# Performance work log

Hardware: AMD Instinct MI355X
Metric: run time of the kernel (lower is better)

## Reference

```python
import jax, jax.numpy as jnp
import numpy as np

HEADS = 16
D_MODEL = 1024
D_K = D_MODEL // HEADS


def setup_inputs() -> dict:
    key = jax.random.key(0)
    ks = jax.random.split(key, 11)
    B, S, D = 4, 2048, D_MODEL
    q = jax.random.normal(ks[0], (B, S, D), dtype=jnp.float32)
    k = jax.random.normal(ks[1], (B, S, D), dtype=jnp.float32)
    v = jax.random.normal(ks[2], (B, S, D), dtype=jnp.float32)
    s = 1.0 / np.sqrt(D)
    Wq = jax.random.normal(ks[3], (D, D), dtype=jnp.float32) * s
    bq = jax.random.normal(ks[4], (D,), dtype=jnp.float32) * 0.01
    Wk = jax.random.normal(ks[5], (D, D), dtype=jnp.float32) * s
    bk = jax.random.normal(ks[6], (D,), dtype=jnp.float32) * 0.01
    Wv = jax.random.normal(ks[7], (D, D), dtype=jnp.float32) * s
    bv = jax.random.normal(ks[8], (D,), dtype=jnp.float32) * 0.01
    Wo = jax.random.normal(ks[9], (D, D), dtype=jnp.float32) * s
    bo = jax.random.normal(ks[10], (D,), dtype=jnp.float32) * 0.01
    return {"q": q, "k": k, "v": v, "Wq": Wq, "bq": bq, "Wk": Wk, "bk": bk,
            "Wv": Wv, "bv": bv, "Wo": Wo, "bo": bo}


def reference(q, k, v, Wq, bq, Wk, bk, Wv, bv, Wo, bo):
    B, Sq, D = q.shape
    Sk = k.shape[1]
    # Linear projections (torch Linear: x @ W.T + b)
    q_ = (q @ Wq.T + bq).reshape(B, Sq, HEADS, D_K).transpose(0, 2, 1, 3)  # [B,H,Sq,Dk]
    k_ = (k @ Wk.T + bk).reshape(B, Sk, HEADS, D_K).transpose(0, 2, 1, 3)  # [B,H,Sk,Dk]
    v_ = (v @ Wv.T + bv).reshape(B, Sk, HEADS, D_K).transpose(0, 2, 1, 3)  # [B,H,Sk,Dk]
    scores = jnp.einsum("bhqd,bhkd->bhqk", q_, k_) / jnp.sqrt(jnp.float32(D_K))
    attn = jax.nn.softmax(scores, axis=-1)
    ctx = jnp.einsum("bhqk,bhkd->bhqd", attn, v_)  # [B,H,Sq,Dk]
    concat = ctx.transpose(0, 2, 1, 3).reshape(B, Sq, D)
    # dropout p=0 -> identity (eval)
    return concat @ Wo.T + bo
```

## Files before the change

### kernel.cpp

```cpp
#include <hip/hip_runtime.h>
#include <hip/hip_bf16.h>
#include <stdint.h>

typedef unsigned short u16;
typedef __attribute__((ext_vector_type(8))) short bf16x8;
typedef __attribute__((ext_vector_type(4))) float f32x4;
typedef __attribute__((ext_vector_type(16))) float f32x16;
typedef __attribute__((ext_vector_type(4))) int i32x4;

#define BATCH 4
#define HEADS 16
#define SEQ   2048
#define DMODEL 1024
#define DK    64
#define QSCALE (0.125f * 1.44269504088896340736f)

__device__ __forceinline__ u16 f2bf(float f) {
  __hip_bfloat16 h = __float2bfloat16(f);
  return *reinterpret_cast<u16*>(&h);
}

__device__ __forceinline__ int cvtpk(float a, float b) {
  int r;
  asm("v_cvt_pk_bf16_f32 %0, %1, %2" : "=v"(r) : "v"(a), "v"(b));
  return r;
}

__device__ __forceinline__ void plswap(int& a, int& b) {
  asm volatile("v_permlane32_swap_b32 %0, %1" : "+v"(a), "+v"(b));
}

__device__ __forceinline__ void gload_lds16(const u16* g, u16* l) {
  __builtin_amdgcn_global_load_lds((const __attribute__((address_space(1))) void*)g,
                                   (__attribute__((address_space(3))) void*)l, 16, 0, 0);
}

__device__ __forceinline__ void sbar() {
  asm volatile("" ::: "memory");
  __builtin_amdgcn_s_barrier();
  __builtin_amdgcn_sched_barrier(0);
}
#define WAITV(N)                                              \
  do {                                                        \
    asm volatile("s_waitcnt vmcnt(" #N ")" ::: "memory");     \
    __builtin_amdgcn_sched_barrier(0);                        \
  } while (0)

__device__ __forceinline__ void cvt8(const float* __restrict__ in, u16* __restrict__ out, long i) {
  float4 a = *(const float4*)(in + i);
  float4 b = *(const float4*)(in + i + 4);
  i32x4 pk;
  pk[0] = cvtpk(a.x, a.y); pk[1] = cvtpk(a.z, a.w);
  pk[2] = cvtpk(b.x, b.y); pk[3] = cvtpk(b.z, b.w);
  *(i32x4*)(out + i) = pk;
}

__global__ void cvt_all(const float* __restrict__ q, const float* __restrict__ k,
                        const float* __restrict__ v, const float* __restrict__ w0,
                        const float* __restrict__ w1, const float* __restrict__ w2,
                        const float* __restrict__ w3, u16* __restrict__ qo,
                        u16* __restrict__ ko, u16* __restrict__ vo,
                        u16* __restrict__ o0, u16* __restrict__ o1,
                        u16* __restrict__ o2, u16* __restrict__ o3) {
  const int sel = blockIdx.y;
  long i = ((long)blockIdx.x * blockDim.x + threadIdx.x) * 8;
  if (sel >= 3 && i >= (long)DMODEL * DMODEL) return;
  const float* in = (sel == 0) ? q : (sel == 1) ? k : (sel == 2) ? v
                  : (sel == 3) ? w0 : (sel == 4) ? w1 : (sel == 5) ? w2 : w3;
  u16* out = (sel == 0) ? qo : (sel == 1) ? ko : (sel == 2) ? vo
           : (sel == 3) ? o0 : (sel == 4) ? o1 : (sel == 5) ? o2 : o3;
  cvt8(in, out, i);
}

__device__ __forceinline__ void gemm_kloop(
    const u16* __restrict__ Ag, const u16* __restrict__ Bg,
    u16* As, u16* Bs, f32x4 acc[4][4],
    const int tid, const int wm, const int wn, const int lr, const int lg) {
  const int K = DMODEL;
  int arow[4], acolc[4], brow2[2], bcol2[2];
#pragma unroll
  for (int j = 0; j < 4; j++) {
    const int c = tid + j * 512;
    arow[j] = c >> 3;
    acolc[j] = ((c & 7) ^ (arow[j] & 7)) * 8;
  }
#pragma unroll
  for (int j = 0; j < 2; j++) {
    const int c = tid + j * 512;
    brow2[j] = c >> 3;
    bcol2[j] = ((c & 7) ^ (brow2[j] & 7)) * 8;
  }

#pragma unroll
  for (int j = 0; j < 4; j++)
    gload_lds16(Ag + (size_t)arow[j] * K + acolc[j], As + (tid + j * 512) * 8);
#pragma unroll
  for (int j = 0; j < 2; j++)
    gload_lds16(Bg + (size_t)brow2[j] * K + bcol2[j], Bs + (tid + j * 512) * 8);
#pragma unroll
  for (int j = 0; j < 4; j++)
    gload_lds16(Ag + (size_t)arow[j] * K + 64 + acolc[j], As + 16384 + (tid + j * 512) * 8);
#pragma unroll
  for (int j = 0; j < 2; j++)
    gload_lds16(Bg + (size_t)brow2[j] * K + 64 + bcol2[j], Bs + 8192 + (tid + j * 512) * 8);
  WAITV(6);
  sbar();

  int m = 0;
  for (int t = 0; t < 16; ++t) {
    u16* Ab = As + m * 16384;
    u16* Bb = Bs + (t & 1) * 8192;
    const int m2 = (m + 2 >= 3) ? m - 1 : m + 2;
    const int k1 = (t + 1) * 64;
    const int k2 = (t + 2) * 64;

    bf16x8 a[4], b[4];
#pragma unroll
    for (int i = 0; i < 4; i++) {
      const int r = wm * 64 + i * 16 + lr;
      a[i] = *(const bf16x8*)&Ab[r * 64 + ((lg ^ (r & 7)) * 8)];
    }
#pragma unroll
    for (int j = 0; j < 4; j++) {
      const int r = wn * 64 + j * 16 + lr;
      b[j] = *(const bf16x8*)&Bb[r * 64 + ((lg ^ (r & 7)) * 8)];
    }
    if (t + 1 < 16) {
      u16* Bd = Bs + ((t + 1) & 1) * 8192;
      gload_lds16(Bg + (size_t)brow2[0] * K + k1 + bcol2[0], Bd + tid * 8);
      gload_lds16(Bg + (size_t)brow2[1] * K + k1 + bcol2[1], Bd + (tid + 512) * 8);
    }
    if (t + 2 < 16) {
      u16* Ad = As + m2 * 16384;
      gload_lds16(Ag + (size_t)arow[0] * K + k2 + acolc[0], Ad + tid * 8);
      gload_lds16(Ag + (size_t)arow[1] * K + k2 + acolc[1], Ad + (tid + 512) * 8);
    }
    sbar();
    __builtin_amdgcn_s_setprio(1);
#pragma unroll
    for (int i = 0; i < 4; i++)
#pragma unroll
      for (int j = 0; j < 4; j++)
        acc[i][j] = __builtin_amdgcn_mfma_f32_16x16x32_bf16(a[i], b[j], acc[i][j], 0, 0, 0);
    __builtin_amdgcn_s_setprio(0);
    sbar();

#pragma unroll
    for (int i = 0; i < 4; i++) {
      const int r = wm * 64 + i * 16 + lr;
      a[i] = *(const bf16x8*)&Ab[r * 64 + (((4 + lg) ^ (r & 7)) * 8)];
    }
#pragma unroll
    for (int j = 0; j < 4; j++) {
      const int r = wn * 64 + j * 16 + lr;
      b[j] = *(const bf16x8*)&Bb[r * 64 + (((4 + lg) ^ (r & 7)) * 8)];
    }
    if (t + 2 < 16) {
      u16* Ad = As + m2 * 16384;
      gload_lds16(Ag + (size_t)arow[2] * K + k2 + acolc[2], Ad + (tid + 1024) * 8);
      gload_lds16(Ag + (size_t)arow[3] * K + k2 + acolc[3], Ad + (tid + 1536) * 8);
    }
    sbar();
    __builtin_amdgcn_s_setprio(1);
#pragma unroll
    for (int i = 0; i < 4; i++)
#pragma unroll
      for (int j = 0; j < 4; j++)
        acc[i][j] = __builtin_amdgcn_mfma_f32_16x16x32_bf16(a[i], b[j], acc[i][j], 0, 0, 0);
    __builtin_amdgcn_s_setprio(0);
    if (t < 14) {
      WAITV(4);
    } else {
      WAITV(0);
    }
    sbar();
    m = (m + 1 >= 3) ? 0 : m + 1;
  }
}

__global__ __launch_bounds__(512, 2)
void gemm8_qkv(const u16* __restrict__ qb, const u16* __restrict__ kb,
               const u16* __restrict__ vb, const u16* __restrict__ Wqb,
               const u16* __restrict__ Wkb, const u16* __restrict__ Wvb,
               const float* __restrict__ bq, const float* __restrict__ bk,
               const float* __restrict__ bv, u16* __restrict__ Qp,
               u16* __restrict__ Kp, u16* __restrict__ Vt) {
  __shared__ __align__(16) u16 smem[65536];
  u16* As = smem;
  u16* Bs = smem + 49152;
  const int tid = threadIdx.x;
  const int lane = tid & 63;
  const int w = tid >> 6;
  const int wm = w >> 1, wn = w & 1;
  const int lr = lane & 15, lg = lane >> 4;

  const int wg = blockIdx.y * 24 + blockIdx.x;
  const int swz = (wg & 7) * 96 + (wg >> 3);
  const int bcolg = swz % 24;
  const int brow = swz / 24;
  const int sel = bcolg >> 3;
  const int bcol = bcolg & 7;

  const u16* A  = (sel == 0) ? qb : (sel == 1) ? kb : vb;
  const u16* Bm = (sel == 0) ? Wqb : (sel == 1) ? Wkb : Wvb;
  const float* bias = (sel == 0) ? bq : (sel == 1) ? bk : bv;

  f32x4 acc[4][4] = {};
  gemm_kloop(A + (size_t)(brow * 256) * DMODEL, Bm + (size_t)(bcol * 128) * DMODEL,
             As, Bs, acc, tid, wm, wn, lr, lg);

  if (sel < 2) {
    u16* Cout = (sel == 0) ? Qp : Kp;
    const float oscale = (sel == 0) ? QSCALE : 1.f;
#pragma unroll
    for (int j = 0; j < 4; j++) {
      const int col = bcol * 128 + wn * 64 + j * 16 + lr;
      const float bv_ = bias[col];
#pragma unroll
      for (int i = 0; i < 4; i++) {
        const int row0 = brow * 256 + wm * 64 + i * 16 + lg * 4;
#pragma unroll
        for (int r = 0; r < 4; r++)
          Cout[(size_t)(row0 + r) * DMODEL + col] = f2bf((acc[i][j][r] + bv_) * oscale);
      }
    }
  } else {
    const int b = brow >> 3;
    const int s0 = (brow & 7) * 256;
    u16* tr = smem;
    __syncthreads();
#pragma unroll
    for (int j = 0; j < 4; j++) {
      const int col = wn * 64 + j * 16 + lr;
      const int xsw = (col & 7) << 3;
      const float bv_ = bias[bcol * 128 + col];
#pragma unroll
      for (int i = 0; i < 4; i++) {
        const int r0 = wm * 64 + i * 16 + lg * 4;
#pragma unroll
        for (int pr = 0; pr < 2; pr++) {
          const float e0 = acc[i][j][pr * 2] + bv_;
          const float e1 = acc[i][j][pr * 2 + 1] + bv_;
          *(int*)&tr[col * 256 + ((r0 + pr * 2) ^ xsw)] = cvtpk(e0, e1);
        }
      }
    }
    __syncthreads();
    const int col = tid >> 2;
    const int part = tid & 3;
    const int xsw = (col & 7) << 3;
    const int c = bcol * 128 + col;
    const int hh = c >> 6, dk = c & 63;
    u16* dst = Vt + (size_t)((b * 16 + hh) * 64 + dk) * SEQ + s0 + part * 64;
#pragma unroll
    for (int jj = 0; jj < 8; jj++) {
      bf16x8 vv = *(const bf16x8*)&tr[col * 256 + ((part * 64 + jj * 8) ^ xsw)];
      *(bf16x8*)(dst + jj * 8) = vv;
    }
  }
}

__global__ __launch_bounds__(512, 2)
void gemm8_bt(const u16* __restrict__ A, const u16* __restrict__ Bm,
              const float* __restrict__ bias, float* __restrict__ Cout) {
  __shared__ __align__(16) u16 smem[65536];
  u16* As = smem;
  u16* Bs = smem + 49152;
  const int tid = threadIdx.x;
  const int lane = tid & 63;
  const int w = tid >> 6;
  const int wm = w >> 1, wn = w & 1;
  const int lr = lane & 15, lg = lane >> 4;

  const int wg = blockIdx.y * 8 + blockIdx.x;
  const int swz = (wg & 7) * 32 + (wg >> 3);
  const int bcol = swz & 7;
  const int brow = swz >> 3;

  f32x4 acc[4][4] = {};
  gemm_kloop(A + (size_t)(brow * 256) * DMODEL, Bm + (size_t)(bcol * 128) * DMODEL,
             As, Bs, acc, tid, wm, wn, lr, lg);

#pragma unroll
  for (int j = 0; j < 4; j++) {
    const int col = bcol * 128 + wn * 64 + j * 16 + lr;
    const float bv_ = bias[col];
#pragma unroll
    for (int i = 0; i < 4; i++) {
      const int row0 = brow * 256 + wm * 64 + i * 16 + lg * 4;
#pragma unroll
      for (int r = 0; r < 4; r++)
        Cout[(size_t)(row0 + r) * DMODEL + col] = acc[i][j][r] + bv_;
    }
  }
}

__device__ __forceinline__ void pack_group(const float* p, int* pw) {
  int W0 = cvtpk(p[0], p[1]);
  int W1 = cvtpk(p[2], p[3]);
  int W2 = cvtpk(p[4], p[5]);
  int W3 = cvtpk(p[6], p[7]);
  plswap(W0, W2);
  plswap(W1, W3);
  pw[0] = W0; pw[1] = W1; pw[2] = W2; pw[3] = W3;
}

__global__ __launch_bounds__(256, 4)
void attn2(const u16* __restrict__ Qp, const u16* __restrict__ Kp,
           const u16* __restrict__ Vt, u16* __restrict__ ctx) {
  __shared__ __align__(16) u16 smem[16384];
  const int tid = threadIdx.x;
  const int lane = tid & 63, w = tid >> 6;
  const int hi = lane >> 5;
  const int l31 = lane & 31;

  const int wg = blockIdx.y * gridDim.x + blockIdx.x;
  const int swz = (wg & 7) * 128 + (wg >> 3);
  const int bh = swz >> 4;
  const int b = bh >> 4, h = bh & 15;
  const int q0 = (swz & 15) * 128 + w * 32;

  const u16* qrow = Qp + (size_t)(b * SEQ + q0 + l31) * DMODEL + h * DK + hi * 8;
  bf16x8 qf[4];
#pragma unroll
  for (int kk = 0; kk < 4; kk++) qf[kk] = *(const bf16x8*)(qrow + kk * 16);

  const int srow = tid >> 3;
  const int scb = tid & 7;
  const int scol = (scb ^ (srow & 7)) * 8;
  const u16* kp = Kp + (size_t)(b * SEQ + srow) * DMODEL + h * DK + scol;
  const u16* vp = Vt + (size_t)bh * DK * SEQ + (size_t)srow * SEQ + scol;

  const int ksw = (l31 & 7) << 3;

  f32x16 o0 = {}, o1 = {};
  float lacc[4] = {};
  const int NT = SEQ / 64;

  {
    u16* Kd = smem;
    u16* Vd = smem + 4096;
    gload_lds16(kp, Kd + tid * 8);
    gload_lds16(kp + 32 * DMODEL, Kd + tid * 8 + 2048);
    gload_lds16(vp, Vd + tid * 8);
    gload_lds16(vp + 32 * SEQ, Vd + tid * 8 + 2048);
    kp += 64 * DMODEL;
    vp += 64;
  }
  __syncthreads();

  for (int t = 0; t < NT; ++t) {
    const int p = t & 1;
    if (t + 1 < NT) {
      u16* Kd = smem + ((p ^ 1) << 13);
      u16* Vd = Kd + 4096;
      gload_lds16(kp, Kd + tid * 8);
      gload_lds16(kp + 32 * DMODEL, Kd + tid * 8 + 2048);
      gload_lds16(vp, Vd + tid * 8);
      gload_lds16(vp + 32 * SEQ, Vd + tid * 8 + 2048);
      kp += 64 * DMODEL;
      vp += 64;
    }

    const u16* Kc = smem + (p << 13);
    const u16* Vc = Kc + 4096;

    f32x16 st0 = {}, st1 = {};
    __builtin_amdgcn_s_setprio(1);
#pragma unroll
    for (int kk = 0; kk < 4; kk++) {
      const int slot = (((kk * 2 + hi) << 3) ^ ksw);
      bf16x8 k0 = *(const bf16x8*)&Kc[l31 * 64 + slot];
      bf16x8 k1 = *(const bf16x8*)&Kc[(l31 + 32) * 64 + slot];
      st0 = __builtin_amdgcn_mfma_f32_32x32x16_bf16(k0, qf[kk], st0, 0, 0, 0);
      st1 = __builtin_amdgcn_mfma_f32_32x32x16_bf16(k1, qf[kk], st1, 0, 0, 0);
    }
    __builtin_amdgcn_s_setprio(0);

#pragma unroll
    for (int i = 0; i < 16; i++) st0[i] = __builtin_amdgcn_exp2f(st0[i]);
#pragma unroll
    for (int i = 0; i < 16; i++) st1[i] = __builtin_amdgcn_exp2f(st1[i]);
    float ts[8];
#pragma unroll
    for (int i = 0; i < 8; i++) ts[i] = (st0[i] + st0[i + 8]) + (st1[i] + st1[i + 8]);
#pragma unroll
    for (int i = 0; i < 4; i++) lacc[i] += ts[i] + ts[i + 4];

    int pw[4][4];
    {
      float tmp[8];
#pragma unroll
      for (int i = 0; i < 8; i++) tmp[i] = st0[i];
      pack_group(tmp, pw[0]);
#pragma unroll
      for (int i = 0; i < 8; i++) tmp[i] = st0[i + 8];
      pack_group(tmp, pw[1]);
#pragma unroll
      for (int i = 0; i < 8; i++) tmp[i] = st1[i];
      pack_group(tmp, pw[2]);
#pragma unroll
      for (int i = 0; i < 8; i++) tmp[i] = st1[i + 8];
      pack_group(tmp, pw[3]);
    }

    __builtin_amdgcn_s_setprio(1);
#pragma unroll
    for (int c = 0; c < 4; c++) {
      i32x4 pwv;
      pwv[0] = pw[c][0]; pwv[1] = pw[c][1]; pwv[2] = pw[c][2]; pwv[3] = pw[c][3];
      bf16x8 pf = __builtin_bit_cast(bf16x8, pwv);
      const int slot = (((c * 2 + hi) << 3) ^ ksw);
      bf16x8 v0 = *(const bf16x8*)&Vc[l31 * 64 + slot];
      bf16x8 v1 = *(const bf16x8*)&Vc[(l31 + 32) * 64 + slot];
      o0 = __builtin_amdgcn_mfma_f32_32x32x16_bf16(v0, pf, o0, 0, 0, 0);
      o1 = __builtin_amdgcn_mfma_f32_32x32x16_bf16(v1, pf, o1, 0, 0, 0);
    }
    __builtin_amdgcn_s_setprio(0);

    __syncthreads();
  }

  float lsum = (lacc[0] + lacc[1]) + (lacc[2] + lacc[3]);
  lsum += __shfl_xor(lsum, 32);
  const float rl = 1.0f / lsum;
  u16* ot = smem + w * (32 * 72);
#pragma unroll
  for (int ds_ = 0; ds_ < 2; ds_++) {
#pragma unroll
    for (int g = 0; g < 4; g++) {
#pragma unroll
      for (int pr = 0; pr < 2; pr++) {
        const int r = g * 4 + pr * 2;
        const int d = ds_ * 32 + (r & 3) + 8 * (r >> 2) + 4 * hi;
        float e0 = (ds_ ? o1[r] : o0[r]) * rl;
        float e1 = (ds_ ? o1[r + 1] : o0[r + 1]) * rl;
        *(int*)&ot[l31 * 72 + d] = cvtpk(e0, e1);
      }
    }
  }
  __syncthreads();
  const int rq = lane >> 3;
  const int rc = (lane & 7) * 8;
#pragma unroll
  for (int it = 0; it < 4; ++it) {
    const int qq = it * 8 + rq;
    bf16x8 vrow = *(const bf16x8*)&ot[qq * 72 + rc];
    *(bf16x8*)&ctx[(size_t)(b * SEQ + q0 + qq) * DMODEL + h * DK + rc] = vrow;
  }
}

extern "C" void kernel_launch(void* const* d_in, const int* in_sizes, int n_in,
                              void* d_out, int out_size, void* d_ws, size_t ws_size,
                              hipStream_t stream) {
  const float* q  = (const float*)d_in[0];
  const float* k  = (const float*)d_in[1];
  const float* v  = (const float*)d_in[2];
  const float* Wq = (const float*)d_in[3];
  const float* bq = (const float*)d_in[4];
  const float* Wk = (const float*)d_in[5];
  const float* bk = (const float*)d_in[6];
  const float* Wv = (const float*)d_in[7];
  const float* bv = (const float*)d_in[8];
  const float* Wo = (const float*)d_in[9];
  const float* bo = (const float*)d_in[10];

  char* ws = (char*)d_ws;
  const size_t MB = 1024 * 1024;
  u16* qb  = (u16*)(ws + 0 * MB);
  u16* kb  = (u16*)(ws + 16 * MB);
  u16* vb  = (u16*)(ws + 32 * MB);
  u16* Wqb = (u16*)(ws + 48 * MB);
  u16* Wkb = (u16*)(ws + 50 * MB);
  u16* Wvb = (u16*)(ws + 52 * MB);
  u16* Wob = (u16*)(ws + 54 * MB);
  u16* Qp  = (u16*)(ws + 56 * MB);
  u16* Kp  = (u16*)(ws + 72 * MB);
  u16* Vt  = (u16*)(ws + 104 * MB);
  u16* ctx = (u16*)(ws + 120 * MB);

  const long nIn = (long)BATCH * SEQ * DMODEL;

  cvt_all<<<dim3(nIn / 8 / 256, 7), 256, 0, stream>>>(q, k, v, Wq, Wk, Wv, Wo,
                                                      qb, kb, vb, Wqb, Wkb, Wvb, Wob);

  gemm8_qkv<<<dim3(24, 32), 512, 0, stream>>>(qb, kb, vb, Wqb, Wkb, Wvb,
                                              bq, bk, bv, Qp, Kp, Vt);

  attn2<<<dim3(16, 64), 256, 0, stream>>>(Qp, Kp, Vt, ctx);

  gemm8_bt<<<dim3(8, 32), 512, 0, stream>>>(ctx, Wob, bo, (float*)d_out);
}
```

Before: 198.8 us.

## Fuse fp32-to-bf16 activation conversion into QKV projection GEMM A-tile loads

The separate pass that converted the q/k/v activations to bf16 is removed. The QKV GEMM now loads fp32 activations into registers, packs them to bf16 and writes them to shared memory itself, using a register-prefetched double buffer in place of the previous 3-stage direct-to-LDS pipeline. Only the weights are still converted in a small standalone kernel. This saves a full read and write of the 48 MB of activations, at the cost of reading fp32 A tiles twice per column-block across the GEMM, and of higher register pressure since launch bounds drop to one block per SM.

```diff
diff --git a/kernel.cpp b/kernel.cpp
--- a/kernel.cpp
+++ b/kernel.cpp
@@ -45,8 +45,20 @@
     asm volatile("s_waitcnt vmcnt(" #N ")" ::: "memory");     \
     __builtin_amdgcn_sched_barrier(0);                        \
   } while (0)
-
-__device__ __forceinline__ void cvt8(const float* __restrict__ in, u16* __restrict__ out, long i) {
+#define WAITLGKM0()                                           \
+  do {                                                        \
+    asm volatile("s_waitcnt lgkmcnt(0)" ::: "memory");        \
+    __builtin_amdgcn_sched_barrier(0);                        \
+  } while (0)
+
+__global__ void cvt_w(const float* __restrict__ w0, const float* __restrict__ w1,
+                      const float* __restrict__ w2, const float* __restrict__ w3,
+                      u16* __restrict__ o0, u16* __restrict__ o1,
+                      u16* __restrict__ o2, u16* __restrict__ o3) {
+  const int sel = blockIdx.y;
+  long i = ((long)blockIdx.x * blockDim.x + threadIdx.x) * 8;
+  const float* in = (sel == 0) ? w0 : (sel == 1) ? w1 : (sel == 2) ? w2 : w3;
+  u16* out = (sel == 0) ? o0 : (sel == 1) ? o1 : (sel == 2) ? o2 : o3;
   float4 a = *(const float4*)(in + i);
   float4 b = *(const float4*)(in + i + 4);
   i32x4 pk;
@@ -55,21 +67,190 @@
   *(i32x4*)(out + i) = pk;
 }
 
-__global__ void cvt_all(const float* __restrict__ q, const float* __restrict__ k,
-                        const float* __restrict__ v, const float* __restrict__ w0,
-                        const float* __restrict__ w1, const float* __restrict__ w2,
-                        const float* __restrict__ w3, u16* __restrict__ qo,
-                        u16* __restrict__ ko, u16* __restrict__ vo,
-                        u16* __restrict__ o0, u16* __restrict__ o1,
-                        u16* __restrict__ o2, u16* __restrict__ o3) {
-  const int sel = blockIdx.y;
-  long i = ((long)blockIdx.x * blockDim.x + threadIdx.x) * 8;
-  if (sel >= 3 && i >= (long)DMODEL * DMODEL) return;
-  const float* in = (sel == 0) ? q : (sel == 1) ? k : (sel == 2) ? v
-                  : (sel == 3) ? w0 : (sel == 4) ? w1 : (sel == 5) ? w2 : w3;
-  u16* out = (sel == 0) ? qo : (sel == 1) ? ko : (sel == 2) ? vo
-           : (sel == 3) ? o0 : (sel == 4) ? o1 : (sel == 5) ? o2 : o3;
-  cvt8(in, out, i);
+__global__ __launch_bounds__(512, 1)
+void gemm8_qkv(const float* __restrict__ qf, const float* __restrict__ kf,
+               const float* __restrict__ vf, const u16* __restrict__ Wqb,
+               const u16* __restrict__ Wkb, const u16* __restrict__ Wvb,
+               const float* __restrict__ bq, const float* __restrict__ bk,
+               const float* __restrict__ bv, u16* __restrict__ Qp,
+               u16* __restrict__ Kp, u16* __restrict__ Vt) {
+  __shared__ __align__(16) u16 smem[49152];
+  u16* As = smem;
+  u16* Bs = smem + 32768;
+  const int K = DMODEL;
+  const int tid = threadIdx.x;
+  const int lane = tid & 63;
+  const int w = tid >> 6;
+  const int wm = w >> 1, wn = w & 1;
+  const int lr = lane & 15, lg = lane >> 4;
+
+  const int wg = blockIdx.y * 24 + blockIdx.x;
+  const int swz = (wg & 7) * 96 + (wg >> 3);
+  const int bcolg = swz % 24;
+  const int brow = swz / 24;
+  const int sel = bcolg >> 3;
+  const int bcol = bcolg & 7;
+
+  const float* Ag = ((sel == 0) ? qf : (sel == 1) ? kf : vf) + (size_t)(brow * 256) * K;
+  const u16* Bg = ((sel == 0) ? Wqb : (sel == 1) ? Wkb : Wvb) + (size_t)(bcol * 128) * K;
+  const float* bias = (sel == 0) ? bq : (sel == 1) ? bk : bv;
+
+  int arow[4], acolc[4], brow2[2], bcol2[2];
+#pragma unroll
+  for (int j = 0; j < 4; j++) {
+    const int c = tid + j * 512;
+    arow[j] = c >> 3;
+    acolc[j] = ((c & 7) ^ (arow[j] & 7)) * 8;
+  }
+#pragma unroll
+  for (int j = 0; j < 2; j++) {
+    const int c = tid + j * 512;
+    brow2[j] = c >> 3;
+    bcol2[j] = ((c & 7) ^ (brow2[j] & 7)) * 8;
+  }
+
+  f32x4 acc[4][4] = {};
+  float4 areg[4][2];
+
+#pragma unroll
+  for (int j = 0; j < 4; j++) {
+    areg[j][0] = *(const float4*)(Ag + (size_t)arow[j] * K + acolc[j]);
+    areg[j][1] = *(const float4*)(Ag + (size_t)arow[j] * K + acolc[j] + 4);
+  }
+#pragma unroll
+  for (int j = 0; j < 2; j++)
+    gload_lds16(Bg + (size_t)brow2[j] * K + bcol2[j], Bs + (tid + j * 512) * 8);
+#pragma unroll
+  for (int j = 0; j < 4; j++) {
+    i32x4 pk;
+    pk[0] = cvtpk(areg[j][0].x, areg[j][0].y);
+    pk[1] = cvtpk(areg[j][0].z, areg[j][0].w);
+    pk[2] = cvtpk(areg[j][1].x, areg[j][1].y);
+    pk[3] = cvtpk(areg[j][1].z, areg[j][1].w);
+    *(i32x4*)(As + (tid + j * 512) * 8) = pk;
+  }
+#pragma unroll
+  for (int j = 0; j < 4; j++) {
+    areg[j][0] = *(const float4*)(Ag + (size_t)arow[j] * K + 64 + acolc[j]);
+    areg[j][1] = *(const float4*)(Ag + (size_t)arow[j] * K + 64 + acolc[j] + 4);
+  }
+  WAITV(8);
+  WAITLGKM0();
+  sbar();
+
+  for (int t = 0; t < 16; ++t) {
+    const int p = t & 1;
+    u16* Ab = As + p * 16384;
+    u16* Bb = Bs + p * 8192;
+
+    if (t < 15) {
+      WAITV(0);
+      u16* Ad = As + (p ^ 1) * 16384;
+#pragma unroll
+      for (int j = 0; j < 4; j++) {
+        i32x4 pk;
+        pk[0] = cvtpk(areg[j][0].x, areg[j][0].y);
+        pk[1] = cvtpk(areg[j][0].z, areg[j][0].w);
+        pk[2] = cvtpk(areg[j][1].x, areg[j][1].y);
+        pk[3] = cvtpk(areg[j][1].z, areg[j][1].w);
+        *(i32x4*)(Ad + (tid + j * 512) * 8) = pk;
+      }
+      u16* Bd = Bs + (p ^ 1) * 8192;
+      const int kb1 = (t + 1) * 64;
+      gload_lds16(Bg + (size_t)brow2[0] * K + kb1 + bcol2[0], Bd + tid * 8);
+      gload_lds16(Bg + (size_t)brow2[1] * K + kb1 + bcol2[1], Bd + (tid + 512) * 8);
+      __builtin_amdgcn_sched_barrier(0);
+      if (t < 14) {
+        const int ka2 = (t + 2) * 64;
+#pragma unroll
+        for (int j = 0; j < 4; j++) {
+          areg[j][0] = *(const float4*)(Ag + (size_t)arow[j] * K + ka2 + acolc[j]);
+          areg[j][1] = *(const float4*)(Ag + (size_t)arow[j] * K + ka2 + acolc[j] + 4);
+        }
+      }
+      __builtin_amdgcn_sched_barrier(0);
+    }
+
+#pragma unroll
+    for (int h = 0; h < 2; h++) {
+      bf16x8 a[4], b[4];
+#pragma unroll
+      for (int i = 0; i < 4; i++) {
+        const int r = wm * 64 + i * 16 + lr;
+        a[i] = *(const bf16x8*)&Ab[r * 64 + (((h * 4 + lg) ^ (r & 7)) * 8)];
+      }
+#pragma unroll
+      for (int j = 0; j < 4; j++) {
+        const int r = wn * 64 + j * 16 + lr;
+        b[j] = *(const bf16x8*)&Bb[r * 64 + (((h * 4 + lg) ^ (r & 7)) * 8)];
+      }
+      __builtin_amdgcn_s_setprio(1);
+#pragma unroll
+      for (int i = 0; i < 4; i++)
+#pragma unroll
+        for (int j = 0; j < 4; j++)
+          acc[i][j] = __builtin_amdgcn_mfma_f32_16x16x32_bf16(a[i], b[j], acc[i][j], 0, 0, 0);
+      __builtin_amdgcn_s_setprio(0);
+    }
+
+    if (t < 14) {
+      WAITV(8);
+    } else {
+      WAITV(0);
+    }
+    WAITLGKM0();
+    sbar();
+  }
+
+  if (sel < 2) {
+    u16* Cout = (sel == 0) ? Qp : Kp;
+    const float oscale = (sel == 0) ? QSCALE : 1.f;
+#pragma unroll
+    for (int j = 0; j < 4; j++) {
+      const int col = bcol * 128 + wn * 64 + j * 16 + lr;
+      const float bv_ = bias[col];
+#pragma unroll
+      for (int i = 0; i < 4; i++) {
+        const int row0 = brow * 256 + wm * 64 + i * 16 + lg * 4;
+#pragma unroll
+        for (int r = 0; r < 4; r++)
+          Cout[(size_t)(row0 + r) * DMODEL + col] = f2bf((acc[i][j][r] + bv_) * oscale);
+      }
+    }
+  } else {
+    const int b = brow >> 3;
+    const int s0 = (brow & 7) * 256;
+    u16* tr = smem;
+    __syncthreads();
+#pragma unroll
+    for (int j = 0; j < 4; j++) {
+      const int col = wn * 64 + j * 16 + lr;
+      const int xsw = (col & 7) << 3;
+      const float bv_ = bias[bcol * 128 + col];
+#pragma unroll
+      for (int i = 0; i < 4; i++) {
+        const int r0 = wm * 64 + i * 16 + lg * 4;
+#pragma unroll
+        for (int pr = 0; pr < 2; pr++) {
+          const float e0 = acc[i][j][pr * 2] + bv_;
+          const float e1 = acc[i][j][pr * 2 + 1] + bv_;
+          *(int*)&tr[col * 256 + ((r0 + pr * 2) ^ xsw)] = cvtpk(e0, e1);
+        }
+      }
+    }
+    __syncthreads();
+    const int col = tid >> 2;
+    const int part = tid & 3;
+    const int xsw = (col & 7) << 3;
+    const int c = bcol * 128 + col;
+    const int hh = c >> 6, dk = c & 63;
+    u16* dst = Vt + (size_t)((b * 16 + hh) * 64 + dk) * SEQ + s0 + part * 64;
+#pragma unroll
+    for (int jj = 0; jj < 8; jj++) {
+      bf16x8 vv = *(const bf16x8*)&tr[col * 256 + ((part * 64 + jj * 8) ^ xsw)];
+      *(bf16x8*)(dst + jj * 8) = vv;
+    }
+  }
 }
 
 __device__ __forceinline__ void gemm_kloop(
@@ -175,88 +356,6 @@
     }
     sbar();
     m = (m + 1 >= 3) ? 0 : m + 1;
-  }
-}
-
-__global__ __launch_bounds__(512, 2)
-void gemm8_qkv(const u16* __restrict__ qb, const u16* __restrict__ kb,
-               const u16* __restrict__ vb, const u16* __restrict__ Wqb,
-               const u16* __restrict__ Wkb, const u16* __restrict__ Wvb,
-               const float* __restrict__ bq, const float* __restrict__ bk,
-               const float* __restrict__ bv, u16* __restrict__ Qp,
-               u16* __restrict__ Kp, u16* __restrict__ Vt) {
-  __shared__ __align__(16) u16 smem[65536];
-  u16* As = smem;
-  u16* Bs = smem + 49152;
-  const int tid = threadIdx.x;
-  const int lane = tid & 63;
-  const int w = tid >> 6;
-  const int wm = w >> 1, wn = w & 1;
-  const int lr = lane & 15, lg = lane >> 4;
-
-  const int wg = blockIdx.y * 24 + blockIdx.x;
-  const int swz = (wg & 7) * 96 + (wg >> 3);
-  const int bcolg = swz % 24;
-  const int brow = swz / 24;
-  const int sel = bcolg >> 3;
-  const int bcol = bcolg & 7;
-
-  const u16* A  = (sel == 0) ? qb : (sel == 1) ? kb : vb;
-  const u16* Bm = (sel == 0) ? Wqb : (sel == 1) ? Wkb : Wvb;
-  const float* bias = (sel == 0) ? bq : (sel == 1) ? bk : bv;
-
-  f32x4 acc[4][4] = {};
-  gemm_kloop(A + (size_t)(brow * 256) * DMODEL, Bm + (size_t)(bcol * 128) * DMODEL,
-             As, Bs, acc, tid, wm, wn, lr, lg);
-
-  if (sel < 2) {
-    u16* Cout = (sel == 0) ? Qp : Kp;
-    const float oscale = (sel == 0) ? QSCALE : 1.f;
-#pragma unroll
-    for (int j = 0; j < 4; j++) {
-      const int col = bcol * 128 + wn * 64 + j * 16 + lr;
-      const float bv_ = bias[col];
-#pragma unroll
-      for (int i = 0; i < 4; i++) {
-        const int row0 = brow * 256 + wm * 64 + i * 16 + lg * 4;
-#pragma unroll
-        for (int r = 0; r < 4; r++)
-          Cout[(size_t)(row0 + r) * DMODEL + col] = f2bf((acc[i][j][r] + bv_) * oscale);
-      }
-    }
-  } else {
-    const int b = brow >> 3;
-    const int s0 = (brow & 7) * 256;
-    u16* tr = smem;
-    __syncthreads();
-#pragma unroll
-    for (int j = 0; j < 4; j++) {
-      const int col = wn * 64 + j * 16 + lr;
-      const int xsw = (col & 7) << 3;
-      const float bv_ = bias[bcol * 128 + col];
-#pragma unroll
-      for (int i = 0; i < 4; i++) {
-        const int r0 = wm * 64 + i * 16 + lg * 4;
-#pragma unroll
-        for (int pr = 0; pr < 2; pr++) {
-          const float e0 = acc[i][j][pr * 2] + bv_;
-          const float e1 = acc[i][j][pr * 2 + 1] + bv_;
-          *(int*)&tr[col * 256 + ((r0 + pr * 2) ^ xsw)] = cvtpk(e0, e1);
-        }
-      }
-    }
-    __syncthreads();
-    const int col = tid >> 2;
-    const int part = tid & 3;
-    const int xsw = (col & 7) << 3;
-    const int c = bcol * 128 + col;
-    const int hh = c >> 6, dk = c & 63;
-    u16* dst = Vt + (size_t)((b * 16 + hh) * 64 + dk) * SEQ + s0 + part * 64;
-#pragma unroll
-    for (int jj = 0; jj < 8; jj++) {
-      bf16x8 vv = *(const bf16x8*)&tr[col * 256 + ((part * 64 + jj * 8) ^ xsw)];
-      *(bf16x8*)(dst + jj * 8) = vv;
-    }
   }
 }
 
@@ -467,9 +566,6 @@
 
   char* ws = (char*)d_ws;
   const size_t MB = 1024 * 1024;
-  u16* qb  = (u16*)(ws + 0 * MB);
-  u16* kb  = (u16*)(ws + 16 * MB);
-  u16* vb  = (u16*)(ws + 32 * MB);
   u16* Wqb = (u16*)(ws + 48 * MB);
   u16* Wkb = (u16*)(ws + 50 * MB);
   u16* Wvb = (u16*)(ws + 52 * MB);
@@ -479,12 +575,11 @@
   u16* Vt  = (u16*)(ws + 104 * MB);
   u16* ctx = (u16*)(ws + 120 * MB);
 
-  const long nIn = (long)BATCH * SEQ * DMODEL;
-
-  cvt_all<<<dim3(nIn / 8 / 256, 7), 256, 0, stream>>>(q, k, v, Wq, Wk, Wv, Wo,
-                                                      qb, kb, vb, Wqb, Wkb, Wvb, Wob);
-
-  gemm8_qkv<<<dim3(24, 32), 512, 0, stream>>>(qb, kb, vb, Wqb, Wkb, Wvb,
+  const long nW = (long)DMODEL * DMODEL;
+
+  cvt_w<<<dim3(nW / 8 / 256, 4), 256, 0, stream>>>(Wq, Wk, Wv, Wo, Wqb, Wkb, Wvb, Wob);
+
+  gemm8_qkv<<<dim3(24, 32), 512, 0, stream>>>(q, k, v, Wqb, Wkb, Wvb,
                                               bq, bk, bv, Qp, Kp, Vt);
 
   attn2<<<dim3(16, 64), 256, 0, stream>>>(Qp, Kp, Vt, ctx);
```

New measurement: 188.7 us. -5.1%, faster.

## Fuse activation fp32-to-bf16 conversion into QKV projection GEMM

Applied to the files above, without the earlier changes.

Drops the separate conversion pass over q, k, v. The QKV GEMM now loads fp32 activations directly, converts them in registers and writes bf16 into LDS, with a simpler double-buffered 128x128 tile kernel. Only the weights are still pre-converted in a small kernel. This removes a full write and re-read of the bf16 activation copies, at the cost of a less tuned GEMM pipeline, register-staged A loads and an unswizzled LDS layout that may cause bank conflicts.

```diff
diff --git a/kernel.cpp b/kernel.cpp
--- a/kernel.cpp
+++ b/kernel.cpp
@@ -46,7 +46,14 @@
     __builtin_amdgcn_sched_barrier(0);                        \
   } while (0)
 
-__device__ __forceinline__ void cvt8(const float* __restrict__ in, u16* __restrict__ out, long i) {
+__global__ void cvt_w(const float* __restrict__ w0, const float* __restrict__ w1,
+                      const float* __restrict__ w2, const float* __restrict__ w3,
+                      u16* __restrict__ o0, u16* __restrict__ o1,
+                      u16* __restrict__ o2, u16* __restrict__ o3) {
+  const int sel = blockIdx.y;
+  long i = ((long)blockIdx.x * blockDim.x + threadIdx.x) * 8;
+  const float* in = (sel == 0) ? w0 : (sel == 1) ? w1 : (sel == 2) ? w2 : w3;
+  u16* out = (sel == 0) ? o0 : (sel == 1) ? o1 : (sel == 2) ? o2 : o3;
   float4 a = *(const float4*)(in + i);
   float4 b = *(const float4*)(in + i + 4);
   i32x4 pk;
@@ -55,21 +62,158 @@
   *(i32x4*)(out + i) = pk;
 }
 
-__global__ void cvt_all(const float* __restrict__ q, const float* __restrict__ k,
-                        const float* __restrict__ v, const float* __restrict__ w0,
-                        const float* __restrict__ w1, const float* __restrict__ w2,
-                        const float* __restrict__ w3, u16* __restrict__ qo,
-                        u16* __restrict__ ko, u16* __restrict__ vo,
-                        u16* __restrict__ o0, u16* __restrict__ o1,
-                        u16* __restrict__ o2, u16* __restrict__ o3) {
-  const int sel = blockIdx.y;
-  long i = ((long)blockIdx.x * blockDim.x + threadIdx.x) * 8;
-  if (sel >= 3 && i >= (long)DMODEL * DMODEL) return;
-  const float* in = (sel == 0) ? q : (sel == 1) ? k : (sel == 2) ? v
-                  : (sel == 3) ? w0 : (sel == 4) ? w1 : (sel == 5) ? w2 : w3;
-  u16* out = (sel == 0) ? qo : (sel == 1) ? ko : (sel == 2) ? vo
-           : (sel == 3) ? o0 : (sel == 4) ? o1 : (sel == 5) ? o2 : o3;
-  cvt8(in, out, i);
+__global__ __launch_bounds__(256, 4)
+void gemm97_qkv(const float* __restrict__ qf, const float* __restrict__ kf,
+                const float* __restrict__ vf, const u16* __restrict__ Wqb,
+                const u16* __restrict__ Wkb, const u16* __restrict__ Wvb,
+                const float* __restrict__ bq, const float* __restrict__ bk,
+                const float* __restrict__ bv, u16* __restrict__ Qp,
+                u16* __restrict__ Kp, u16* __restrict__ Vt) {
+  __shared__ __align__(16) u16 smem[16384];
+  u16* As = smem;
+  u16* Bs = smem + 8192;
+  const int K = DMODEL;
+  const int tid = threadIdx.x;
+  const int lane = tid & 63;
+  const int w = tid >> 6;
+  const int wm = w >> 1, wn = w & 1;
+  const int lr = lane & 15, lg = lane >> 4;
+
+  const int wg = blockIdx.y * 24 + blockIdx.x;
+  const int swz = (wg & 7) * 192 + (wg >> 3);
+  const int bcolg = swz % 24;
+  const int brow = swz / 24;
+  const int sel = bcolg >> 3;
+  const int bcol = bcolg & 7;
+
+  const float* Ag = ((sel == 0) ? qf : (sel == 1) ? kf : vf) + (size_t)(brow * 128) * K;
+  const u16* Bg = ((sel == 0) ? Wqb : (sel == 1) ? Wkb : Wvb) + (size_t)(bcol * 128) * K;
+  const float* bias = (sel == 0) ? bq : (sel == 1) ? bk : bv;
+
+  const int r0_ = tid >> 2;
+  const int cc_ = (tid & 3) * 8;
+
+  f32x4 acc[4][4] = {};
+  float4 areg[2][2];
+
+  areg[0][0] = *(const float4*)(Ag + (size_t)r0_ * K + cc_);
+  areg[0][1] = *(const float4*)(Ag + (size_t)r0_ * K + cc_ + 4);
+  areg[1][0] = *(const float4*)(Ag + (size_t)(r0_ + 64) * K + cc_);
+  areg[1][1] = *(const float4*)(Ag + (size_t)(r0_ + 64) * K + cc_ + 4);
+#pragma unroll
+  for (int j = 0; j < 2; j++) {
+    i32x4 pk;
+    pk[0] = cvtpk(areg[j][0].x, areg[j][0].y);
+    pk[1] = cvtpk(areg[j][0].z, areg[j][0].w);
+    pk[2] = cvtpk(areg[j][1].x, areg[j][1].y);
+    pk[3] = cvtpk(areg[j][1].z, areg[j][1].w);
+    *(i32x4*)(As + (tid + j * 256) * 8) = pk;
+  }
+  gload_lds16(Bg + (size_t)r0_ * K + cc_, Bs + tid * 8);
+  gload_lds16(Bg + (size_t)(r0_ + 64) * K + cc_, Bs + (tid + 256) * 8);
+  areg[0][0] = *(const float4*)(Ag + (size_t)r0_ * K + 32 + cc_);
+  areg[0][1] = *(const float4*)(Ag + (size_t)r0_ * K + 32 + cc_ + 4);
+  areg[1][0] = *(const float4*)(Ag + (size_t)(r0_ + 64) * K + 32 + cc_);
+  areg[1][1] = *(const float4*)(Ag + (size_t)(r0_ + 64) * K + 32 + cc_ + 4);
+  __syncthreads();
+
+  const int NT = 32;
+  for (int t = 0; t < NT; ++t) {
+    const int p = t & 1;
+    const u16* Ab = As + p * 4096;
+    const u16* Bb = Bs + p * 4096;
+
+    if (t + 1 < NT) {
+      u16* Ad = As + (p ^ 1) * 4096;
+#pragma unroll
+      for (int j = 0; j < 2; j++) {
+        i32x4 pk;
+        pk[0] = cvtpk(areg[j][0].x, areg[j][0].y);
+        pk[1] = cvtpk(areg[j][0].z, areg[j][0].w);
+        pk[2] = cvtpk(areg[j][1].x, areg[j][1].y);
+        pk[3] = cvtpk(areg[j][1].z, areg[j][1].w);
+        *(i32x4*)(Ad + (tid + j * 256) * 8) = pk;
+      }
+      u16* Bd = Bs + (p ^ 1) * 4096;
+      const int k1 = (t + 1) * 32;
+      gload_lds16(Bg + (size_t)r0_ * K + k1 + cc_, Bd + tid * 8);
+      gload_lds16(Bg + (size_t)(r0_ + 64) * K + k1 + cc_, Bd + (tid + 256) * 8);
+      if (t + 2 < NT) {
+        const int k2 = (t + 2) * 32;
+        areg[0][0] = *(const float4*)(Ag + (size_t)r0_ * K + k2 + cc_);
+        areg[0][1] = *(const float4*)(Ag + (size_t)r0_ * K + k2 + cc_ + 4);
+        areg[1][0] = *(const float4*)(Ag + (size_t)(r0_ + 64) * K + k2 + cc_);
+        areg[1][1] = *(const float4*)(Ag + (size_t)(r0_ + 64) * K + k2 + cc_ + 4);
+      }
+    }
+
+    bf16x8 a[4], b[4];
+#pragma unroll
+    for (int i = 0; i < 4; i++)
+      a[i] = *(const bf16x8*)&Ab[(wm * 64 + i * 16 + lr) * 32 + lg * 8];
+#pragma unroll
+    for (int j = 0; j < 4; j++)
+      b[j] = *(const bf16x8*)&Bb[(wn * 64 + j * 16 + lr) * 32 + lg * 8];
+    __builtin_amdgcn_s_setprio(1);
+#pragma unroll
+    for (int i = 0; i < 4; i++)
+#pragma unroll
+      for (int j = 0; j < 4; j++)
+        acc[i][j] = __builtin_amdgcn_mfma_f32_16x16x32_bf16(a[i], b[j], acc[i][j], 0, 0, 0);
+    __builtin_amdgcn_s_setprio(0);
+
+    __syncthreads();
+  }
+
+  if (sel < 2) {
+    u16* Cout = (sel == 0) ? Qp : Kp;
+    const float oscale = (sel == 0) ? QSCALE : 1.f;
+#pragma unroll
+    for (int j = 0; j < 4; j++) {
+      const int col = bcol * 128 + wn * 64 + j * 16 + lr;
+      const float bv_ = bias[col];
+#pragma unroll
+      for (int i = 0; i < 4; i++) {
+        const int row0 = brow * 128 + wm * 64 + i * 16 + lg * 4;
+#pragma unroll
+        for (int r = 0; r < 4; r++)
+          Cout[(size_t)(row0 + r) * DMODEL + col] = f2bf((acc[i][j][r] + bv_) * oscale);
+      }
+    }
+  } else {
+    const int b = brow >> 4;
+    const int s0 = (brow & 15) * 128;
+    u16* tr = smem;
+    __syncthreads();
+#pragma unroll
+    for (int j = 0; j < 4; j++) {
+      const int col = wn * 64 + j * 16 + lr;
+      const int xsw = (col & 7) << 3;
+      const float bv_ = bias[bcol * 128 + col];
+#pragma unroll
+      for (int i = 0; i < 4; i++) {
+        const int rr0 = wm * 64 + i * 16 + lg * 4;
+#pragma unroll
+        for (int pr = 0; pr < 2; pr++) {
+          const float e0 = acc[i][j][pr * 2] + bv_;
+          const float e1 = acc[i][j][pr * 2 + 1] + bv_;
+          *(int*)&tr[col * 128 + ((rr0 + pr * 2) ^ xsw)] = cvtpk(e0, e1);
+        }
+      }
+    }
+    __syncthreads();
+    const int col = tid >> 1;
+    const int part = tid & 1;
+    const int xsw = (col & 7) << 3;
+    const int c = bcol * 128 + col;
+    const int hh = c >> 6, dk = c & 63;
+    u16* dst = Vt + (size_t)((b * 16 + hh) * 64 + dk) * SEQ + s0 + part * 64;
+#pragma unroll
+    for (int jj = 0; jj < 8; jj++) {
+      bf16x8 vv = *(const bf16x8*)&tr[col * 128 + ((part * 64 + jj * 8) ^ xsw)];
+      *(bf16x8*)(dst + jj * 8) = vv;
+    }
+  }
 }
 
 __device__ __forceinline__ void gemm_kloop(
@@ -175,88 +319,6 @@
     }
     sbar();
     m = (m + 1 >= 3) ? 0 : m + 1;
-  }
-}
-
-__global__ __launch_bounds__(512, 2)
-void gemm8_qkv(const u16* __restrict__ qb, const u16* __restrict__ kb,
-               const u16* __restrict__ vb, const u16* __restrict__ Wqb,
-               const u16* __restrict__ Wkb, const u16* __restrict__ Wvb,
-               const float* __restrict__ bq, const float* __restrict__ bk,
-               const float* __restrict__ bv, u16* __restrict__ Qp,
-               u16* __restrict__ Kp, u16* __restrict__ Vt) {
-  __shared__ __align__(16) u16 smem[65536];
-  u16* As = smem;
-  u16* Bs = smem + 49152;
-  const int tid = threadIdx.x;
-  const int lane = tid & 63;
-  const int w = tid >> 6;
-  const int wm = w >> 1, wn = w & 1;
-  const int lr = lane & 15, lg = lane >> 4;
-
-  const int wg = blockIdx.y * 24 + blockIdx.x;
-  const int swz = (wg & 7) * 96 + (wg >> 3);
-  const int bcolg = swz % 24;
-  const int brow = swz / 24;
-  const int sel = bcolg >> 3;
-  const int bcol = bcolg & 7;
-
-  const u16* A  = (sel == 0) ? qb : (sel == 1) ? kb : vb;
-  const u16* Bm = (sel == 0) ? Wqb : (sel == 1) ? Wkb : Wvb;
-  const float* bias = (sel == 0) ? bq : (sel == 1) ? bk : bv;
-
-  f32x4 acc[4][4] = {};
-  gemm_kloop(A + (size_t)(brow * 256) * DMODEL, Bm + (size_t)(bcol * 128) * DMODEL,
-             As, Bs, acc, tid, wm, wn, lr, lg);
-
-  if (sel < 2) {
-    u16* Cout = (sel == 0) ? Qp : Kp;
-    const float oscale = (sel == 0) ? QSCALE : 1.f;
-#pragma unroll
-    for (int j = 0; j < 4; j++) {
-      const int col = bcol * 128 + wn * 64 + j * 16 + lr;
-      const float bv_ = bias[col];
-#pragma unroll
-      for (int i = 0; i < 4; i++) {
-        const int row0 = brow * 256 + wm * 64 + i * 16 + lg * 4;
-#pragma unroll
-        for (int r = 0; r < 4; r++)
-          Cout[(size_t)(row0 + r) * DMODEL + col] = f2bf((acc[i][j][r] + bv_) * oscale);
-      }
-    }
-  } else {
-    const int b = brow >> 3;
-    const int s0 = (brow & 7) * 256;
-    u16* tr = smem;
-    __syncthreads();
-#pragma unroll
-    for (int j = 0; j < 4; j++) {
-      const int col = wn * 64 + j * 16 + lr;
-      const int xsw = (col & 7) << 3;
-      const float bv_ = bias[bcol * 128 + col];
-#pragma unroll
-      for (int i = 0; i < 4; i++) {
-        const int r0 = wm * 64 + i * 16 + lg * 4;
-#pragma unroll
-        for (int pr = 0; pr < 2; pr++) {
-          const float e0 = acc[i][j][pr * 2] + bv_;
-          const float e1 = acc[i][j][pr * 2 + 1] + bv_;
-          *(int*)&tr[col * 256 + ((r0 + pr * 2) ^ xsw)] = cvtpk(e0, e1);
-        }
-      }
-    }
-    __syncthreads();
-    const int col = tid >> 2;
-    const int part = tid & 3;
-    const int xsw = (col & 7) << 3;
-    const int c = bcol * 128 + col;
-    const int hh = c >> 6, dk = c & 63;
-    u16* dst = Vt + (size_t)((b * 16 + hh) * 64 + dk) * SEQ + s0 + part * 64;
-#pragma unroll
-    for (int jj = 0; jj < 8; jj++) {
-      bf16x8 vv = *(const bf16x8*)&tr[col * 256 + ((part * 64 + jj * 8) ^ xsw)];
-      *(bf16x8*)(dst + jj * 8) = vv;
-    }
   }
 }
 
@@ -467,9 +529,6 @@
 
   char* ws = (char*)d_ws;
   const size_t MB = 1024 * 1024;
-  u16* qb  = (u16*)(ws + 0 * MB);
-  u16* kb  = (u16*)(ws + 16 * MB);
-  u16* vb  = (u16*)(ws + 32 * MB);
   u16* Wqb = (u16*)(ws + 48 * MB);
   u16* Wkb = (u16*)(ws + 50 * MB);
   u16* Wvb = (u16*)(ws + 52 * MB);
@@ -479,13 +538,12 @@
   u16* Vt  = (u16*)(ws + 104 * MB);
   u16* ctx = (u16*)(ws + 120 * MB);
 
-  const long nIn = (long)BATCH * SEQ * DMODEL;
-
-  cvt_all<<<dim3(nIn / 8 / 256, 7), 256, 0, stream>>>(q, k, v, Wq, Wk, Wv, Wo,
-                                                      qb, kb, vb, Wqb, Wkb, Wvb, Wob);
-
-  gemm8_qkv<<<dim3(24, 32), 512, 0, stream>>>(qb, kb, vb, Wqb, Wkb, Wvb,
-                                              bq, bk, bv, Qp, Kp, Vt);
+  const long nW = (long)DMODEL * DMODEL;
+
+  cvt_w<<<dim3(nW / 8 / 256, 4), 256, 0, stream>>>(Wq, Wk, Wv, Wo, Wqb, Wkb, Wvb, Wob);
+
+  gemm97_qkv<<<dim3(24, 64), 256, 0, stream>>>(q, k, v, Wqb, Wkb, Wvb,
+                                               bq, bk, bv, Qp, Kp, Vt);
 
   attn2<<<dim3(16, 64), 256, 0, stream>>>(Qp, Kp, Vt, ctx);
 
```

After: 188.9 us. 1.05x faster.
